# Kernel optimization log

Measured on AMD Instinct MI355X. Metric: run time of the kernel, lower is better.

The kernel has to match this reference:

```python
import jax, jax.numpy as jnp
import numpy as np

LEVEL = 0.1
SEED = 12345
RAND_MAX = 4294967295.0
BN_EPS = 1e-5


def lcg_noise(n):
    # Original: seed_{t+1} = (65539*seed_t + 1) & 0xFFFFFFFF; value_t = seed_{t+1}/RAND_MAX
    # Closed form: seed_{t+1} = M^{t+1} * s0 + sum_{k=0}^{t} M^k  (mod 2^32).
    # uint32 arithmetic wraps mod 2^32, so cumprod/cumsum give exact jump-ahead.
    m = jnp.full((n,), 65539, dtype=jnp.uint32)
    powers = jnp.cumprod(m)  # M^1 .. M^n (mod 2^32)
    geom = jnp.cumsum(jnp.concatenate([jnp.ones((1,), jnp.uint32), powers[:-1]]))  # sum_{k=0}^{t} M^k
    seeds = powers * jnp.uint32(SEED) + geom  # wraps mod 2^32
    return seeds.astype(jnp.float32) * jnp.float32(LEVEL / RAND_MAX)


def setup_inputs() -> dict:
    key = jax.random.key(0)
    k1, k2 = jax.random.split(key)
    B, Cin, Cout, H, W = 32, 256, 512, 64, 64
    x = jax.random.normal(k1, (B, Cin, H, W), dtype=jnp.float32)
    conv_w = jax.random.normal(k2, (Cout, Cin), dtype=jnp.float32) * 0.02
    conv_b = jnp.zeros((Cout,), dtype=jnp.float32)
    gamma = jnp.ones((Cout,), dtype=jnp.float32)
    beta = jnp.zeros((Cout,), dtype=jnp.float32)
    return {"x": x, "conv_w": conv_w, "conv_b": conv_b, "gamma": gamma, "beta": beta}


def reference(x, conv_w, conv_b, gamma, beta):
    B, C, H, W = x.shape
    noise = lcg_noise(C * H * W).reshape(C, H, W)  # batch-independent, broadcast over B
    x2 = jax.nn.relu(x + noise[None])
    # 1x1 conv == per-pixel GEMM
    y = jnp.einsum('bchw,oc->bohw', x2, conv_w) + conv_b[None, :, None, None]
    # BatchNorm2d (training mode: batch statistics, biased variance)
    mean = jnp.mean(y, axis=(0, 2, 3))
    var = jnp.var(y, axis=(0, 2, 3))
    y_hat = (y - mean[None, :, None, None]) * jax.lax.rsqrt(var + BN_EPS)[None, :, None, None]
    return y_hat * gamma[None, :, None, None] + beta[None, :, None, None]
```

## Files before the change

### kernel.cpp

```cpp
#include <hip/hip_runtime.h>
#include <cstdint>

#define B_    32
#define CIN   256
#define COUT  512
#define HW    4096
#define NPIX  (B_ * HW)
#define NOISE_N (CIN * HW)
#define WN    (COUT * CIN)

typedef _Float16 f16;
typedef _Float16 f16x8 __attribute__((ext_vector_type(8)));
typedef float    f32x4 __attribute__((ext_vector_type(4)));

__device__ __forceinline__ unsigned lcg_seed_after(unsigned n) {
  unsigned A = 1u, Bc = 0u;
  unsigned mA = 65539u, mB = 1u;
  #pragma unroll
  for (int i = 0; i < 21; ++i) {
    if (n & (1u << i)) { A = mA * A; Bc = mA * Bc + mB; }
    mB = mA * mB + mB;
    mA = mA * mA;
  }
  return A * 12345u + Bc;
}

__global__ void k_prep(const float* __restrict__ conv_w,
                       float* __restrict__ noise, f16* __restrict__ w2) {
  const int tid = blockIdx.x * 256 + threadIdx.x;
  if (tid < NOISE_N) {
    const unsigned seed = lcg_seed_after((unsigned)tid + 1u);
    noise[tid] = (float)seed * (float)(0.1 / 4294967295.0);
  } else {
    const int i = tid - NOISE_N;
    if (i < WN) w2[i] = (f16)conv_w[i];
  }
}

__device__ __forceinline__ int tadr(int c, int chunk) {
  return (c << 6) + (((chunk ^ ((c >> 1) & 3)) & 3) << 4);
}

__global__ __launch_bounds__(1024) void k1_gram(
    const float* __restrict__ x, const float* __restrict__ noise,
    f16* __restrict__ x2t, float* __restrict__ gpart,
    float* __restrict__ sums, int npart, int useAtomic) {
  __shared__ unsigned char sm[32768];
  const int t = threadIdx.x;
  const int lane = t & 63;
  const int w = t >> 6;
  const int wm = w >> 2, wn = w & 3;
  const int bid = blockIdx.x;
  const int b = bid >> 3;
  const int hw0 = (bid & 7) << 9;

  const int cL = t >> 2;
  const int pq = t & 3;
  const int p0 = pq << 3;
  const float* xrow = x + (((size_t)(b * CIN + cL)) << 12) + hw0 + p0;
  const float* nrow = noise + (((size_t)cL) << 12) + hw0 + p0;
  const int wbyte = tadr(cL, pq);

  const int tp = t & 31;
  const int c0 = (t >> 5) << 3;

  f32x4 acc[4][4];
  #pragma unroll
  for (int i = 0; i < 4; ++i)
    #pragma unroll
    for (int j = 0; j < 4; ++j)
      acc[i][j] = (f32x4){0.f, 0.f, 0.f, 0.f};
  float csum = 0.f;

  {
    const float4 xa = *(const float4*)(xrow);
    const float4 xb = *(const float4*)(xrow + 4);
    const float4 na = *(const float4*)(nrow);
    const float4 nb = *(const float4*)(nrow + 4);
    f16x8 hv;
    hv[0] = (f16)fmaxf(xa.x + na.x, 0.f); hv[1] = (f16)fmaxf(xa.y + na.y, 0.f);
    hv[2] = (f16)fmaxf(xa.z + na.z, 0.f); hv[3] = (f16)fmaxf(xa.w + na.w, 0.f);
    hv[4] = (f16)fmaxf(xb.x + nb.x, 0.f); hv[5] = (f16)fmaxf(xb.y + nb.y, 0.f);
    hv[6] = (f16)fmaxf(xb.z + nb.z, 0.f); hv[7] = (f16)fmaxf(xb.w + nb.w, 0.f);
    #pragma unroll
    for (int i = 0; i < 8; ++i) csum += (float)hv[i];
    *(f16x8*)(sm + wbyte) = hv;
  }
  __syncthreads();

  for (int s = 0; s < 16; ++s) {
    const int base = (s & 1) << 14;
    float4 xa, xb;
    if (s < 15) {
      xa = *(const float4*)(xrow + (s + 1) * 32);
      xb = *(const float4*)(xrow + (s + 1) * 32 + 4);
    }
    {
      const int ch = lane >> 4;
      f16x8 af[4];
      #pragma unroll
      for (int mi = 0; mi < 4; ++mi)
        af[mi] = *(const f16x8*)(sm + base + tadr(wm * 64 + mi * 16 + (lane & 15), ch));
      #pragma unroll
      for (int ni = 0; ni < 4; ++ni) {
        const f16x8 bf = *(const f16x8*)(sm + base + tadr(wn * 64 + ni * 16 + (lane & 15), ch));
        #pragma unroll
        for (int mi = 0; mi < 4; ++mi)
          acc[mi][ni] = __builtin_amdgcn_mfma_f32_16x16x32_f16(af[mi], bf, acc[mi][ni], 0, 0, 0);
      }
    }
    uint4 pk;
    {
      unsigned short vals[8];
      #pragma unroll
      for (int j = 0; j < 8; ++j) {
        const int row = c0 + j;
        const int addr = base + (row << 6) + ((2 * tp) & 15) +
                         ((((tp >> 3) ^ ((row >> 1) & 3)) & 3) << 4);
        vals[j] = *(const unsigned short*)(sm + addr);
      }
      pk.x = (unsigned)vals[0] | ((unsigned)vals[1] << 16);
      pk.y = (unsigned)vals[2] | ((unsigned)vals[3] << 16);
      pk.z = (unsigned)vals[4] | ((unsigned)vals[5] << 16);
      pk.w = (unsigned)vals[6] | ((unsigned)vals[7] << 16);
    }
    if (s < 15) {
      const float4 na = *(const float4*)(nrow + (s + 1) * 32);
      const float4 nb = *(const float4*)(nrow + (s + 1) * 32 + 4);
      f16x8 hv;
      hv[0] = (f16)fmaxf(xa.x + na.x, 0.f); hv[1] = (f16)fmaxf(xa.y + na.y, 0.f);
      hv[2] = (f16)fmaxf(xa.z + na.z, 0.f); hv[3] = (f16)fmaxf(xa.w + na.w, 0.f);
      hv[4] = (f16)fmaxf(xb.x + nb.x, 0.f); hv[5] = (f16)fmaxf(xb.y + nb.y, 0.f);
      hv[6] = (f16)fmaxf(xb.z + nb.z, 0.f); hv[7] = (f16)fmaxf(xb.w + nb.w, 0.f);
      #pragma unroll
      for (int i = 0; i < 8; ++i) csum += (float)hv[i];
      *(f16x8*)(sm + (base ^ 16384) + wbyte) = hv;
    }
    __syncthreads();
    *(uint4*)((char*)x2t + ((size_t)(b * HW + hw0 + s * 32 + tp)) * 512 + (c0 << 1)) = pk;
  }

  {
    float* gp = gpart + (size_t)(bid % npart) * 65536;
    if (useAtomic) {
      #pragma unroll
      for (int mi = 0; mi < 4; ++mi)
        #pragma unroll
        for (int ni = 0; ni < 4; ++ni)
          #pragma unroll
          for (int r = 0; r < 4; ++r) {
            const int m = 64 * wm + 16 * mi + 4 * (lane >> 4) + r;
            const int n = 64 * wn + 16 * ni + (lane & 15);
            atomicAdd(&gp[m * 256 + n], acc[mi][ni][r]);
          }
    } else {
      #pragma unroll
      for (int mi = 0; mi < 4; ++mi)
        #pragma unroll
        for (int ni = 0; ni < 4; ++ni)
          #pragma unroll
          for (int r = 0; r < 4; ++r) {
            const int m = 64 * wm + 16 * mi + 4 * (lane >> 4) + r;
            const int n = 64 * wn + 16 * ni + (lane & 15);
            gp[m * 256 + n] = acc[mi][ni][r];
          }
    }
  }
  {
    float* sl = (float*)sm;
    sl[(cL << 2) + pq] = csum;
    __syncthreads();
    if (t < 256) {
      const float* r4 = sl + (t << 2);
      atomicAdd(&sums[t], (r4[0] + r4[1]) + (r4[2] + r4[3]));
    }
  }
}

__global__ void k_greduce(const float* __restrict__ gpart, float* __restrict__ G, int npart) {
  const int i = blockIdx.x * 256 + threadIdx.x;
  float s0 = 0.f, s1 = 0.f, s2 = 0.f, s3 = 0.f;
  int k = 0;
  for (; k + 4 <= npart; k += 4) {
    s0 += gpart[(size_t)(k + 0) * 65536 + i];
    s1 += gpart[(size_t)(k + 1) * 65536 + i];
    s2 += gpart[(size_t)(k + 2) * 65536 + i];
    s3 += gpart[(size_t)(k + 3) * 65536 + i];
  }
  for (; k < npart; ++k) s0 += gpart[(size_t)k * 65536 + i];
  G[i] = (s0 + s1) + (s2 + s3);
}

__global__ __launch_bounds__(256) void k_stats(
    const float* __restrict__ G, const float* __restrict__ sums,
    const f16* __restrict__ w2, const float* __restrict__ gamma,
    const float* __restrict__ beta, float* __restrict__ scale,
    float* __restrict__ shift) {
  const int o = blockIdx.x, c = threadIdx.x;
  const float wc = (float)w2[o * 256 + c];
  const float4* G4 = (const float4*)(G + (c << 8));
  const f16* wr = w2 + o * 256;
  float tc = 0.f;
  #pragma unroll 4
  for (int j8 = 0; j8 < 32; ++j8) {
    const f16x8 wv = *(const f16x8*)(wr + j8 * 8);
    const float4 ga = G4[2 * j8], gb = G4[2 * j8 + 1];
    tc += ga.x * (float)wv[0] + ga.y * (float)wv[1] + ga.z * (float)wv[2] + ga.w * (float)wv[3]
        + gb.x * (float)wv[4] + gb.y * (float)wv[5] + gb.z * (float)wv[6] + gb.w * (float)wv[7];
  }
  float q = wc * tc;
  float uv = wc * sums[c];
  #pragma unroll
  for (int off = 32; off > 0; off >>= 1) {
    q  += __shfl_down(q, off);
    uv += __shfl_down(uv, off);
  }
  __shared__ float rq[4], ru[4];
  const int lane = c & 63, w = c >> 6;
  if (lane == 0) { rq[w] = q; ru[w] = uv; }
  __syncthreads();
  if (c == 0) {
    const float Q = rq[0] + rq[1] + rq[2] + rq[3];
    const float U = ru[0] + ru[1] + ru[2] + ru[3];
    const float invN = 1.f / (float)NPIX;
    const float u = U * invN;
    const float var = Q * invN - u * u;
    const float sc = gamma[o] * rsqrtf(var + 1e-5f);
    scale[o] = sc;
    shift[o] = beta[o] - u * sc;
  }
}

__global__ __launch_bounds__(256) void k_gemm(
    const f16* __restrict__ w2, const f16* __restrict__ x2t,
    const float* __restrict__ scale, const float* __restrict__ shift,
    float* __restrict__ out) {
  __shared__ unsigned char sm[65536];
  const int t = threadIdx.x, lane = t & 63, w = t >> 6;
  const int wm = w >> 1, wn = w & 1;
  const int bid = (blockIdx.x & 7) * 512 + (blockIdx.x >> 3);
  const int ot = bid & 3;
  const int pt = bid >> 2;
  const int b = pt >> 5;
  const int hw0 = (pt & 31) << 7;
  const int o0 = ot << 7;
  const size_t gp0 = (size_t)b * HW + hw0;

  f32x4 acc[4][4];
  #pragma unroll
  for (int i = 0; i < 4; ++i)
    #pragma unroll
    for (int j = 0; j < 4; ++j)
      acc[i][j] = (f32x4){0.f, 0.f, 0.f, 0.f};

  const int r  = lane >> 3;
  const int cb = (lane & 7) << 4;
  const int cbs = cb ^ (r << 4);

  #define STAGE(kt, buf)                                                          \
    {                                                                             \
      const int bb = (buf) << 15;                                                 \
      _Pragma("unroll")                                                           \
      for (int it = 0; it < 4; ++it) {                                            \
        const int idx = it * 4 + w;                                               \
        const int row = idx * 8 + r;                                              \
        const char* sa = (const char*)w2 + (size_t)(o0 + row) * 512 + (kt) * 128 + cbs; \
        __builtin_amdgcn_global_load_lds(                                         \
            (const __attribute__((address_space(1))) void*)sa,                    \
            (__attribute__((address_space(3))) void*)(sm + bb + idx * 1024), 16, 0, 0); \
        const char* sb = (const char*)x2t + (gp0 + row) * 512 + (kt) * 128 + cbs; \
        __builtin_amdgcn_global_load_lds(                                         \
            (const __attribute__((address_space(1))) void*)sb,                    \
            (__attribute__((address_space(3))) void*)(sm + bb + 16384 + idx * 1024), 16, 0, 0); \
      }                                                                           \
    }

  STAGE(0, 0);
  __syncthreads();
  for (int kt = 0; kt < 4; ++kt) {
    if (kt < 3) STAGE(kt + 1, (kt + 1) & 1);
    const int base = (kt & 1) << 15;
    #pragma unroll
    for (int ks = 0; ks < 2; ++ks) {
      const int kb = 64 * ks + 16 * (lane >> 4);
      f16x8 af[4];
      #pragma unroll
      for (int mi = 0; mi < 4; ++mi) {
        const int rowa = 64 * wm + 16 * mi + (lane & 15);
        af[mi] = *(const f16x8*)(sm + base + rowa * 128 + (kb ^ ((rowa & 7) << 4)));
      }
      #pragma unroll
      for (int ni = 0; ni < 4; ++ni) {
        const int rowb = 64 * wn + 16 * ni + (lane & 15);
        const f16x8 bf = *(const f16x8*)(sm + base + 16384 + rowb * 128 + (kb ^ ((rowb & 7) << 4)));
        #pragma unroll
        for (int mi = 0; mi < 4; ++mi)
          acc[mi][ni] = __builtin_amdgcn_mfma_f32_16x16x32_f16(af[mi], bf, acc[mi][ni], 0, 0, 0);
      }
    }
    __syncthreads();
  }
  #undef STAGE

  #pragma unroll
  for (int mi = 0; mi < 4; ++mi) {
    #pragma unroll
    for (int rr = 0; rr < 4; ++rr) {
      const int o = o0 + 64 * wm + 16 * mi + 4 * (lane >> 4) + rr;
      const float sc = scale[o], sh = shift[o];
      #pragma unroll
      for (int ni = 0; ni < 4; ++ni) {
        const int hw = hw0 + 64 * wn + 16 * ni + (lane & 15);
        out[(((size_t)(b * COUT + o)) << 12) + hw] = acc[mi][ni][rr] * sc + sh;
      }
    }
  }
}

extern "C" void kernel_launch(void* const* d_in, const int* in_sizes, int n_in,
                              void* d_out, int out_size, void* d_ws, size_t ws_size,
                              hipStream_t stream) {
  (void)in_sizes; (void)n_in; (void)out_size;
  const float* x      = (const float*)d_in[0];
  const float* conv_w = (const float*)d_in[1];
  const float* gamma  = (const float*)d_in[3];
  const float* beta   = (const float*)d_in[4];
  float* out = (float*)d_out;
  char* ws = (char*)d_ws;

  float* noise = (float*)(ws);
  float* G     = (float*)(ws + (4u << 20));
  f16*   w2    = (f16*)  (ws + (4u << 20) + (256u << 10));
  float* sums  = (float*)(ws + (4u << 20) + (512u << 10));
  float* scale = (float*)(ws + (4u << 20) + (514u << 10));
  float* shift = (float*)(ws + (4u << 20) + (517u << 10));
  f16*   x2t   = (f16*)  (ws + (5u << 20));
  float* gpart = (float*)(ws + (69u << 20));

  const size_t avail = ws_size > (69ull << 20) ? ws_size - (69ull << 20) : 0;
  int npart = (int)(avail / (65536ull * sizeof(float)));
  if (npart > 256) npart = 256;
  if (npart < 1) npart = 1;
  const int useAtomic = (npart < 256) ? 1 : 0;

  hipMemsetAsync(sums, 0, 256 * sizeof(float), stream);
  if (useAtomic)
    hipMemsetAsync(gpart, 0, (size_t)npart * 65536 * sizeof(float), stream);

  k_prep   <<<4608, 256,  0, stream>>>(conv_w, noise, w2);
  k1_gram  <<<256,  1024, 0, stream>>>(x, noise, x2t, gpart, sums, npart, useAtomic);
  k_greduce<<<256,  256,  0, stream>>>(gpart, G, npart);
  k_stats  <<<COUT, 256,  0, stream>>>(G, sums, w2, gamma, beta, scale, shift);
  k_gemm   <<<4096, 256,  0, stream>>>(w2, x2t, scale, shift, out);
}
```

Before: 491.8 us.

## Generate LCG noise inline in gram kernel and split Gram reduction across blocks

Removes the separate prep kernel: the LCG noise is now computed on the fly inside the gram kernel, using a jump-ahead seed per thread and sequential LCG steps, so the noise buffer is no longer written and re-read. The fp16 weight conversion moves into the Gram partial-reduction kernel. That kernel now splits the partition sum over 8 blocks in y and accumulates into G with atomics, which requires G to be zeroed first. The trade is extra integer work in the gram kernel and float atomics on G, in exchange for one less launch and about 4 MB less global traffic.

```diff
diff --git a/kernel.cpp b/kernel.cpp
--- a/kernel.cpp
+++ b/kernel.cpp
@@ -6,12 +6,12 @@
 #define COUT  512
 #define HW    4096
 #define NPIX  (B_ * HW)
-#define NOISE_N (CIN * HW)
-#define WN    (COUT * CIN)
 
 typedef _Float16 f16;
 typedef _Float16 f16x8 __attribute__((ext_vector_type(8)));
 typedef float    f32x4 __attribute__((ext_vector_type(4)));
+
+#define NSCALE ((float)(0.1 / 4294967295.0))
 
 __device__ __forceinline__ unsigned lcg_seed_after(unsigned n) {
   unsigned A = 1u, Bc = 0u;
@@ -25,24 +25,17 @@
   return A * 12345u + Bc;
 }
 
-__global__ void k_prep(const float* __restrict__ conv_w,
-                       float* __restrict__ noise, f16* __restrict__ w2) {
-  const int tid = blockIdx.x * 256 + threadIdx.x;
-  if (tid < NOISE_N) {
-    const unsigned seed = lcg_seed_after((unsigned)tid + 1u);
-    noise[tid] = (float)seed * (float)(0.1 / 4294967295.0);
-  } else {
-    const int i = tid - NOISE_N;
-    if (i < WN) w2[i] = (f16)conv_w[i];
-  }
-}
+constexpr unsigned lcgA(int k) { unsigned a = 1u; for (int i = 0; i < k; ++i) a *= 65539u; return a; }
+constexpr unsigned lcgC(int k) { unsigned c = 0u; for (int i = 0; i < k; ++i) c = 65539u * c + 1u; return c; }
+constexpr unsigned LCG_A32 = lcgA(32);
+constexpr unsigned LCG_C32 = lcgC(32);
 
 __device__ __forceinline__ int tadr(int c, int chunk) {
   return (c << 6) + (((chunk ^ ((c >> 1) & 3)) & 3) << 4);
 }
 
 __global__ __launch_bounds__(1024) void k1_gram(
-    const float* __restrict__ x, const float* __restrict__ noise,
+    const float* __restrict__ x,
     f16* __restrict__ x2t, float* __restrict__ gpart,
     float* __restrict__ sums, int npart, int useAtomic) {
   __shared__ unsigned char sm[32768];
@@ -58,8 +51,9 @@
   const int pq = t & 3;
   const int p0 = pq << 3;
   const float* xrow = x + (((size_t)(b * CIN + cL)) << 12) + hw0 + p0;
-  const float* nrow = noise + (((size_t)cL) << 12) + hw0 + p0;
   const int wbyte = tadr(cL, pq);
+
+  unsigned sb = lcg_seed_after((unsigned)(cL * HW + hw0 + p0) + 1u);
 
   const int tp = t & 31;
   const int c0 = (t >> 5) << 3;
@@ -75,15 +69,18 @@
   {
     const float4 xa = *(const float4*)(xrow);
     const float4 xb = *(const float4*)(xrow + 4);
-    const float4 na = *(const float4*)(nrow);
-    const float4 nb = *(const float4*)(nrow + 4);
+    float xr[8];
+    xr[0] = xa.x; xr[1] = xa.y; xr[2] = xa.z; xr[3] = xa.w;
+    xr[4] = xb.x; xr[5] = xb.y; xr[6] = xb.z; xr[7] = xb.w;
+    unsigned sj = sb;
     f16x8 hv;
-    hv[0] = (f16)fmaxf(xa.x + na.x, 0.f); hv[1] = (f16)fmaxf(xa.y + na.y, 0.f);
-    hv[2] = (f16)fmaxf(xa.z + na.z, 0.f); hv[3] = (f16)fmaxf(xa.w + na.w, 0.f);
-    hv[4] = (f16)fmaxf(xb.x + nb.x, 0.f); hv[5] = (f16)fmaxf(xb.y + nb.y, 0.f);
-    hv[6] = (f16)fmaxf(xb.z + nb.z, 0.f); hv[7] = (f16)fmaxf(xb.w + nb.w, 0.f);
-    #pragma unroll
-    for (int i = 0; i < 8; ++i) csum += (float)hv[i];
+    #pragma unroll
+    for (int j = 0; j < 8; ++j) {
+      hv[j] = (f16)fmaxf(fmaf((float)sj, NSCALE, xr[j]), 0.f);
+      csum += (float)hv[j];
+      sj = 65539u * sj + 1u;
+    }
+    sb = LCG_A32 * sb + LCG_C32;
     *(f16x8*)(sm + wbyte) = hv;
   }
   __syncthreads();
@@ -125,15 +122,18 @@
       pk.w = (unsigned)vals[6] | ((unsigned)vals[7] << 16);
     }
     if (s < 15) {
-      const float4 na = *(const float4*)(nrow + (s + 1) * 32);
-      const float4 nb = *(const float4*)(nrow + (s + 1) * 32 + 4);
+      float xr[8];
+      xr[0] = xa.x; xr[1] = xa.y; xr[2] = xa.z; xr[3] = xa.w;
+      xr[4] = xb.x; xr[5] = xb.y; xr[6] = xb.z; xr[7] = xb.w;
+      unsigned sj = sb;
       f16x8 hv;
-      hv[0] = (f16)fmaxf(xa.x + na.x, 0.f); hv[1] = (f16)fmaxf(xa.y + na.y, 0.f);
-      hv[2] = (f16)fmaxf(xa.z + na.z, 0.f); hv[3] = (f16)fmaxf(xa.w + na.w, 0.f);
-      hv[4] = (f16)fmaxf(xb.x + nb.x, 0.f); hv[5] = (f16)fmaxf(xb.y + nb.y, 0.f);
-      hv[6] = (f16)fmaxf(xb.z + nb.z, 0.f); hv[7] = (f16)fmaxf(xb.w + nb.w, 0.f);
-      #pragma unroll
-      for (int i = 0; i < 8; ++i) csum += (float)hv[i];
+      #pragma unroll
+      for (int j = 0; j < 8; ++j) {
+        hv[j] = (f16)fmaxf(fmaf((float)sj, NSCALE, xr[j]), 0.f);
+        csum += (float)hv[j];
+        sj = 65539u * sj + 1u;
+      }
+      sb = LCG_A32 * sb + LCG_C32;
       *(f16x8*)(sm + (base ^ 16384) + wbyte) = hv;
     }
     __syncthreads();
@@ -177,18 +177,29 @@
   }
 }
 
-__global__ void k_greduce(const float* __restrict__ gpart, float* __restrict__ G, int npart) {
+__global__ __launch_bounds__(256) void k_greduce(
+    const float* __restrict__ gpart, float* __restrict__ G,
+    const float* __restrict__ conv_w, f16* __restrict__ w2, int npart) {
   const int i = blockIdx.x * 256 + threadIdx.x;
+  const int nk = (npart + 7) >> 3;
+  const int k0 = blockIdx.y * nk;
+  int k1e = k0 + nk; if (k1e > npart) k1e = npart;
   float s0 = 0.f, s1 = 0.f, s2 = 0.f, s3 = 0.f;
-  int k = 0;
-  for (; k + 4 <= npart; k += 4) {
+  int k = k0;
+  for (; k + 4 <= k1e; k += 4) {
     s0 += gpart[(size_t)(k + 0) * 65536 + i];
     s1 += gpart[(size_t)(k + 1) * 65536 + i];
     s2 += gpart[(size_t)(k + 2) * 65536 + i];
     s3 += gpart[(size_t)(k + 3) * 65536 + i];
   }
-  for (; k < npart; ++k) s0 += gpart[(size_t)k * 65536 + i];
-  G[i] = (s0 + s1) + (s2 + s3);
+  for (; k < k1e; ++k) s0 += gpart[(size_t)k * 65536 + i];
+  atomicAdd(&G[i], (s0 + s1) + (s2 + s3));
+  if (blockIdx.y == 0) {
+    const float2 wv = *(const float2*)(conv_w + 2 * i);
+    union { f16 h[2]; unsigned u; } p;
+    p.h[0] = (f16)wv.x; p.h[1] = (f16)wv.y;
+    *(unsigned*)(w2 + 2 * i) = p.u;
+  }
 }
 
 __global__ __launch_bounds__(256) void k_stats(
@@ -328,28 +339,26 @@
   float* out = (float*)d_out;
   char* ws = (char*)d_ws;
 
-  float* noise = (float*)(ws);
-  float* G     = (float*)(ws + (4u << 20));
-  f16*   w2    = (f16*)  (ws + (4u << 20) + (256u << 10));
-  float* sums  = (float*)(ws + (4u << 20) + (512u << 10));
-  float* scale = (float*)(ws + (4u << 20) + (514u << 10));
-  float* shift = (float*)(ws + (4u << 20) + (517u << 10));
-  f16*   x2t   = (f16*)  (ws + (5u << 20));
-  float* gpart = (float*)(ws + (69u << 20));
-
-  const size_t avail = ws_size > (69ull << 20) ? ws_size - (69ull << 20) : 0;
+  float* G     = (float*)(ws);
+  float* sums  = (float*)(ws + 262144);
+  float* scale = (float*)(ws + 263168);
+  float* shift = (float*)(ws + 265216);
+  f16*   w2    = (f16*)  (ws + 267264);
+  f16*   x2t   = (f16*)  (ws + (1u << 20));
+  float* gpart = (float*)(ws + (65u << 20));
+
+  const size_t avail = ws_size > (65ull << 20) ? ws_size - (65ull << 20) : 0;
   int npart = (int)(avail / (65536ull * sizeof(float)));
   if (npart > 256) npart = 256;
   if (npart < 1) npart = 1;
   const int useAtomic = (npart < 256) ? 1 : 0;
 
-  hipMemsetAsync(sums, 0, 256 * sizeof(float), stream);
+  hipMemsetAsync(ws, 0, 263168, stream);
   if (useAtomic)
     hipMemsetAsync(gpart, 0, (size_t)npart * 65536 * sizeof(float), stream);
 
-  k_prep   <<<4608, 256,  0, stream>>>(conv_w, noise, w2);
-  k1_gram  <<<256,  1024, 0, stream>>>(x, noise, x2t, gpart, sums, npart, useAtomic);
-  k_greduce<<<256,  256,  0, stream>>>(gpart, G, npart);
-  k_stats  <<<COUT, 256,  0, stream>>>(G, sums, w2, gamma, beta, scale, shift);
-  k_gemm   <<<4096, 256,  0, stream>>>(w2, x2t, scale, shift, out);
-}
+  k1_gram  <<<256, 1024, 0, stream>>>(x, x2t, gpart, sums, npart, useAtomic);
+  k_greduce<<<dim3(256, 8), 256, 0, stream>>>(gpart, G, conv_w, w2, npart);
+  k_stats  <<<COUT, 256, 0, stream>>>(G, sums, w2, gamma, beta, scale, shift);
+  k_gemm   <<<4096, 256, 0, stream>>>(w2, x2t, scale, shift, out);
+}
```

Result: no change. 484.0 us (-1.6%).
